# Kernel optimization log

Measured on AMD Instinct MI355X. Metric: run time of the kernel, lower is better.

Reference implementation:

```python
import jax, jax.numpy as jnp
import numpy as np

B = 16          # graphs per batch
N_PER = 1024    # coarse points per graph
M_PER = 4096    # fine (skip) points per graph
K = 3           # knn neighbors
NVEC = 64       # number of l=1 (vector) reps -> F = 3*NVEC
F = 3 * NVEC
F_SKIP = 64
HID = 256
OUT = 128
N = B * N_PER
M = B * M_PER


def _random_rotations(key, n):
    # QR of gaussian -> orthonormal local frames [n,3,3]
    q, _ = jnp.linalg.qr(jax.random.normal(key, (n, 3, 3), dtype=jnp.float32))
    return q


def setup_inputs() -> dict:
    key = jax.random.key(0)
    ks = jax.random.split(key, 10)
    x = jax.random.normal(ks[0], (N, F), dtype=jnp.float32)
    pos = jax.random.normal(ks[1], (N, 3), dtype=jnp.float32)
    pos_skip = jax.random.normal(ks[2], (M, 3), dtype=jnp.float32)
    x_skip = jax.random.normal(ks[3], (M, F_SKIP), dtype=jnp.float32)
    lframes = _random_rotations(ks[4], N)
    lframes_skip = _random_rotations(ks[5], M)
    W1 = jax.random.normal(ks[6], (F + F_SKIP, HID), dtype=jnp.float32) * 0.05
    b1 = jnp.zeros((HID,), dtype=jnp.float32)
    W2 = jax.random.normal(ks[7], (HID, OUT), dtype=jnp.float32) * 0.05
    b2 = jnp.zeros((OUT,), dtype=jnp.float32)
    batch = jnp.repeat(jnp.arange(B, dtype=jnp.int64), N_PER)
    batch_skip = jnp.repeat(jnp.arange(B, dtype=jnp.int64), M_PER)
    return dict(x=x, pos=pos, pos_skip=pos_skip, x_skip=x_skip,
                lframes=lframes, lframes_skip=lframes_skip,
                W1=W1, b1=b1, W2=W2, b2=b2,
                batch=batch, batch_skip=batch_skip)


def _knn_indices(pos, pos_skip):
    # Uniform per-example batching: knn of fine points (queries) among coarse points.
    px = pos.reshape(B, N_PER, 3)       # source points
    py = pos_skip.reshape(B, M_PER, 3)  # query points
    # squared distances via ||y||^2 + ||x||^2 - 2 y.x (only used for ranking)
    d2 = ((py * py).sum(-1)[:, :, None]
          + (px * px).sum(-1)[:, None, :]
          - 2.0 * jnp.einsum('bmd,bnd->bmn', py, px))  # [B, M_PER, N_PER]
    _, idx = jax.lax.top_k(-d2, K)                     # [B, M_PER, K] local indices
    # globalize indices (batch offset)
    x_idx = (idx + (jnp.arange(B) * N_PER)[:, None, None]).reshape(M, K)
    return x_idx


def reference(x, pos, pos_skip, x_skip, lframes, lframes_skip,
              W1, b1, W2, b2, batch, batch_skip):
    x_idx = _knn_indices(pos, pos_skip)                 # [M, K]

    # exact squared distances on gathered neighbors (matches torch diff*diff path)
    diff = pos[x_idx] - pos_skip[:, None, :]            # [M, K, 3]
    sqd = (diff * diff).sum(-1)                         # [M, K]
    w = 1.0 / jnp.maximum(sqd, 1e-16)                   # [M, K]

    # change of local frames: U = R_end @ R_start^T, per edge
    Rx = lframes[x_idx]                                 # [M, K, 3, 3]
    Ry = lframes_skip                                   # [M, 3, 3]
    U = jnp.einsum('mab,mkcb->mkac', Ry, Rx)            # [M, K, 3, 3]

    # transform features (NVEC vector reps) into the target frame
    xv = x[x_idx].reshape(M, K, NVEC, 3)                # gathered edge features
    xt = jnp.einsum('mkab,mkvb->mkva', U, xv)           # [M, K, NVEC, 3]

    # weighted mean over the K neighbors (== scatter-sum / scatter-sum, since
    # each target node has exactly K incoming edges)
    num = (xt * w[:, :, None, None]).sum(axis=1)        # [M, NVEC, 3]
    den = w.sum(axis=1)[:, None, None]                  # [M, 1, 1]
    y = (num / den).reshape(M, F)

    h = jnp.concatenate([y, x_skip], axis=-1)           # [M, F + F_SKIP]
    out = jax.nn.relu(h @ W1 + b1) @ W2 + b2            # [M, OUT]
    return (out, pos_skip, batch_skip, lframes_skip)
```

## Files before the change

### kernel.cpp

```cpp
#include <hip/hip_runtime.h>
#include <hip/hip_bf16.h>

#define B_GR   16
#define N_PER  1024
#define M_PER  4096
#define NVEC   64
#define FDIM   192
#define FSKIP  64
#define HID    256
#define ODIM   128
#define N_TOT  (B_GR * N_PER)
#define M_TOT  (B_GR * M_PER)

typedef __attribute__((ext_vector_type(8))) short short8v;
typedef __attribute__((ext_vector_type(4))) float f32x4;

__device__ __forceinline__ unsigned short f2bf(float f) {
    __hip_bfloat16 h = __float2bfloat16(f);
    return *reinterpret_cast<unsigned short*>(&h);
}

__device__ __forceinline__ int hsw(int r, int e) {
    return r * 256 + (e ^ ((r & 7) << 3));
}

__global__ __launch_bounds__(256) void wprep_kernel(
    const float* __restrict__ W1, const float* __restrict__ W2,
    unsigned short* __restrict__ wt1, unsigned short* __restrict__ wt2)
{
    const int i = blockIdx.x * 256 + threadIdx.x;
    if (i < 256 * 256) {
        const int k = i >> 8, c = i & 255;
        wt1[c * 256 + k] = f2bf(W1[i]);
    } else {
        const int j = i - 256 * 256;
        const int k = j >> 7, c = j & 127;
        wt2[c * 256 + k] = f2bf(W2[j]);
    }
}

__global__ __launch_bounds__(512, 2) void fused_kernel(
    const float* __restrict__ x,
    const float* __restrict__ pos,
    const float* __restrict__ pos_skip,
    const float* __restrict__ x_skip,
    const float* __restrict__ lframes,
    const float* __restrict__ lframes_skip,
    const unsigned short* __restrict__ wt1,
    const float* __restrict__ b1,
    const unsigned short* __restrict__ wt2,
    const float* __restrict__ b2,
    float* __restrict__ out)
{
    __shared__ __align__(16) char smraw[64 * 256 * 2];
    __shared__ __align__(16) float Usc[64 * 28];
    __shared__ int idxL[64 * 3];

    float4*         pc = reinterpret_cast<float4*>(smraw);
    unsigned short* hb = reinterpret_cast<unsigned short*>(smraw);

    const int tid  = threadIdx.x;
    const int lane = tid & 63;
    const int wv   = tid >> 6;
    const int raw  = blockIdx.x;
    const int blk  = (raw & 7) * 128 + (raw >> 3);
    const int lo   = lane & 15;
    const int hi   = lane >> 4;
    const int b    = blk >> 6;

    #pragma unroll
    for (int k = 0; k < 2; ++k) {
        const int j = tid + k * 512;
        const float* p = pos + (size_t)(b * N_PER + j) * 3;
        float a0 = p[0], a1 = p[1], a2 = p[2];
        pc[j] = make_float4(a0, a1, a2, a0*a0 + a1*a1 + a2*a2);
    }
    __syncthreads();

    {
        const int q   = tid >> 3;
        const int sub = tid & 7;
        const int m   = blk * 64 + q;
        float nqx, nqy, nqz, qq;
        {
            const float qx = pos_skip[m*3+0], qy = pos_skip[m*3+1],
                        qz = pos_skip[m*3+2];
            qq  = qx*qx + qy*qy + qz*qz;
            nqx = -2.0f*qx; nqy = -2.0f*qy; nqz = -2.0f*qz;
        }

        float d0 = 1e30f, d1 = 1e30f, d2 = 1e30f;
        int   i0 = 0,     i1 = 0,     i2 = 0;
        float e0 = 1e30f, e1 = 1e30f, e2 = 1e30f;
        int   k0 = 0,     k1 = 0,     k2 = 0;
        #pragma unroll 4
        for (int t = 0; t < 64; ++t) {
            const int ja = t*16 + sub;
            const int jb = ja + 8;
            float4 ca = pc[ja];
            float4 cb = pc[jb];
            float ra = fmaf(nqx, ca.x, fmaf(nqy, ca.y, fmaf(nqz, ca.z, qq + ca.w)));
            float rb = fmaf(nqx, cb.x, fmaf(nqy, cb.y, fmaf(nqz, cb.z, qq + cb.w)));
            {
                bool c0 = ra < d0, c1 = ra < d1, c2 = ra < d2;
                i2 = c2 ? (c1 ? i1 : ja) : i2;
                i1 = c1 ? (c0 ? i0 : ja) : i1;
                i0 = c0 ? ja : i0;
                d2 = c2 ? (c1 ? d1 : ra) : d2;
                d1 = c1 ? (c0 ? d0 : ra) : d1;
                d0 = c0 ? ra : d0;
            }
            {
                bool c0 = rb < e0, c1 = rb < e1, c2 = rb < e2;
                k2 = c2 ? (c1 ? k1 : jb) : k2;
                k1 = c1 ? (c0 ? k0 : jb) : k1;
                k0 = c0 ? jb : k0;
                e2 = c2 ? (c1 ? e1 : rb) : e2;
                e1 = c1 ? (c0 ? e0 : rb) : e1;
                e0 = c0 ? rb : e0;
            }
        }
        {
            const float ee[3] = {e0, e1, e2};
            const int   jj[3] = {k0, k1, k2};
            #pragma unroll
            for (int s = 0; s < 3; ++s) {
                const float e = ee[s]; const int j = jj[s];
                bool c0 = (e < d0) || (e == d0 && j < i0);
                bool c1 = (e < d1) || (e == d1 && j < i1);
                bool c2 = (e < d2) || (e == d2 && j < i2);
                i2 = c2 ? (c1 ? i1 : j) : i2;
                i1 = c1 ? (c0 ? i0 : j) : i1;
                i0 = c0 ? j : i0;
                d2 = c2 ? (c1 ? d1 : e) : d2;
                d1 = c1 ? (c0 ? d0 : e) : d1;
                d0 = c0 ? e : d0;
            }
        }
        #pragma unroll
        for (int mask = 1; mask <= 4; mask <<= 1) {
            float f0 = __shfl_xor(d0, mask), f1 = __shfl_xor(d1, mask),
                  f2 = __shfl_xor(d2, mask);
            int   j0 = __shfl_xor(i0, mask), j1 = __shfl_xor(i1, mask),
                  j2 = __shfl_xor(i2, mask);
            const float ee[3] = {f0, f1, f2};
            const int   jj[3] = {j0, j1, j2};
            #pragma unroll
            for (int s = 0; s < 3; ++s) {
                const float e = ee[s]; const int j = jj[s];
                bool c0 = (e < d0) || (e == d0 && j < i0);
                bool c1 = (e < d1) || (e == d1 && j < i1);
                bool c2 = (e < d2) || (e == d2 && j < i2);
                i2 = c2 ? (c1 ? i1 : j) : i2;
                i1 = c1 ? (c0 ? i0 : j) : i1;
                i0 = c0 ? j : i0;
                d2 = c2 ? (c1 ? d1 : e) : d2;
                d1 = c1 ? (c0 ? d0 : e) : d1;
                d0 = c0 ? e : d0;
            }
        }

        if (sub < 3) {
            const int jl = (sub == 0) ? i0 : (sub == 1) ? i1 : i2;
            idxL[q*3 + sub] = jl;

            const float qx = -0.5f*nqx, qy = -0.5f*nqy, qz = -0.5f*nqz;
            float w[3];
            const int jls[3] = {i0, i1, i2};
            #pragma unroll
            for (int s = 0; s < 3; ++s) {
                float4 c = pc[jls[s]];
                float dx = c.x - qx, dy = c.y - qy, dz = c.z - qz;
                w[s] = 1.0f / fmaxf(dx*dx + dy*dy + dz*dz, 1e-16f);
            }
            const float wsub = (sub == 0) ? w[0] : (sub == 1) ? w[1] : w[2];
            const float sS   = wsub / (w[0] + w[1] + w[2]);
            const int   nb   = b * N_PER + jl;

            float RyS[9], Rx[9];
            #pragma unroll
            for (int t = 0; t < 9; ++t) RyS[t] = sS * lframes_skip[(size_t)m*9 + t];
            #pragma unroll
            for (int t = 0; t < 9; ++t) Rx[t] = lframes[(size_t)nb*9 + t];

            float* dst = &Usc[q*28 + sub*9];
            #pragma unroll
            for (int a = 0; a < 3; ++a)
                #pragma unroll
                for (int c = 0; c < 3; ++c)
                    dst[a*3+c] = RyS[a*3+0]*Rx[c*3+0]
                               + RyS[a*3+1]*Rx[c*3+1]
                               + RyS[a*3+2]*Rx[c*3+2];
        }
    }

    if (wv >= 4) {
        #pragma unroll
        for (int rr = 0; rr < 8; ++rr) {
            const int r = wv * 8 + rr;
            const int m = blk * 64 + r;
            hb[hsw(r, 192+lane)] = f2bf(x_skip[(size_t)m*FSKIP + lane]);
        }
    }
    __syncthreads();

    for (int rr = 0; rr < 8; ++rr) {
        const int r = wv * 8 + rr;
        const int m = blk * 64 + r;
        const int nbs[3] = {b*N_PER + idxL[r*3+0],
                            b*N_PER + idxL[r*3+1],
                            b*N_PER + idxL[r*3+2]};

        float Ub[28];
        float4* Ub4 = reinterpret_cast<float4*>(Ub);
        #pragma unroll
        for (int t = 0; t < 7; ++t)
            Ub4[t] = *reinterpret_cast<const float4*>(&Usc[r*28 + t*4]);

        float n0 = 0.f, n1 = 0.f, n2 = 0.f;
        #pragma unroll
        for (int k = 0; k < 3; ++k) {
            const float* xp = x + (size_t)nbs[k]*FDIM + lane*3;
            const float v0 = xp[0], v1 = xp[1], v2 = xp[2];
            const int o = k*9;
            n0 += Ub[o+0]*v0 + Ub[o+1]*v1 + Ub[o+2]*v2;
            n1 += Ub[o+3]*v0 + Ub[o+4]*v1 + Ub[o+5]*v2;
            n2 += Ub[o+6]*v0 + Ub[o+7]*v1 + Ub[o+8]*v2;
        }
        hb[hsw(r, lane*3+0)] = f2bf(n0);
        hb[hsw(r, lane*3+1)] = f2bf(n1);
        hb[hsw(r, lane*3+2)] = f2bf(n2);
        if (wv < 4)
            hb[hsw(r, 192+lane)] = f2bf(x_skip[(size_t)m*FSKIP + lane]);
    }
    __syncthreads();

    f32x4 acc[4][2];
    #pragma unroll
    for (int fi = 0; fi < 4; ++fi)
        #pragma unroll
        for (int ci = 0; ci < 2; ++ci) acc[fi][ci] = (f32x4)0.f;

    for (int ks = 0; ks < 8; ++ks) {
        const int kk = ks*32 + hi*8;
        short8v a[4], bf[2];
        #pragma unroll
        for (int fi = 0; fi < 4; ++fi) {
            const int r = fi*16 + lo;
            a[fi] = *reinterpret_cast<const short8v*>(
                &hb[r*256 + (kk ^ ((lo & 7) << 3))]);
        }
        #pragma unroll
        for (int ci = 0; ci < 2; ++ci) {
            const int cb = wv*32 + ci*16 + lo;
            bf[ci] = *reinterpret_cast<const short8v*>(&wt1[cb*256 + kk]);
        }
        #pragma unroll
        for (int fi = 0; fi < 4; ++fi)
            #pragma unroll
            for (int ci = 0; ci < 2; ++ci)
                acc[fi][ci] = __builtin_amdgcn_mfma_f32_16x16x32_bf16(
                    a[fi], bf[ci], acc[fi][ci], 0, 0, 0);
    }
    __syncthreads();

    {
        float b1v[2];
        #pragma unroll
        for (int ci = 0; ci < 2; ++ci) b1v[ci] = b1[wv*32 + ci*16 + lo];
        #pragma unroll
        for (int fi = 0; fi < 4; ++fi)
            #pragma unroll
            for (int ci = 0; ci < 2; ++ci)
                #pragma unroll
                for (int q = 0; q < 4; ++q) {
                    const int r = fi*16 + hi*4 + q;
                    const int c = wv*32 + ci*16 + lo;
                    hb[hsw(r, c)] = f2bf(fmaxf(acc[fi][ci][q] + b1v[ci], 0.f));
                }
    }
    __syncthreads();

    f32x4 acc2[4];
    #pragma unroll
    for (int fi = 0; fi < 4; ++fi) acc2[fi] = (f32x4)0.f;

    for (int ks = 0; ks < 8; ++ks) {
        const int kk = ks*32 + hi*8;
        short8v a[4], bf;
        #pragma unroll
        for (int fi = 0; fi < 4; ++fi) {
            const int r = fi*16 + lo;
            a[fi] = *reinterpret_cast<const short8v*>(
                &hb[r*256 + (kk ^ ((lo & 7) << 3))]);
        }
        {
            const int cb = wv*16 + lo;
            bf = *reinterpret_cast<const short8v*>(&wt2[cb*256 + kk]);
        }
        #pragma unroll
        for (int fi = 0; fi < 4; ++fi)
            acc2[fi] = __builtin_amdgcn_mfma_f32_16x16x32_bf16(
                a[fi], bf, acc2[fi], 0, 0, 0);
    }

    {
        const float b2v = b2[wv*16 + lo];
        #pragma unroll
        for (int fi = 0; fi < 4; ++fi)
            #pragma unroll
            for (int q = 0; q < 4; ++q) {
                const int r = fi*16 + hi*4 + q;
                const int c = wv*16 + lo;
                out[(size_t)(blk*64 + r)*ODIM + c] = acc2[fi][q] + b2v;
            }
    }
}

__global__ __launch_bounds__(256) void tail_kernel(
    const float* __restrict__ pos_skip,
    const int*   __restrict__ batch_skip,
    const float* __restrict__ lframes_skip,
    float* __restrict__ dst)
{
    const int i = blockIdx.x * 256 + threadIdx.x;
    const int P = M_TOT * 3;
    const int Q = P + M_TOT;
    const int R = Q + M_TOT * 9;
    if (i < P)      dst[i] = pos_skip[i];
    else if (i < Q) dst[i] = (float)batch_skip[i - P];
    else if (i < R) dst[i] = lframes_skip[i - Q];
}

extern "C" void kernel_launch(void* const* d_in, const int* in_sizes, int n_in,
                              void* d_out, int out_size, void* d_ws, size_t ws_size,
                              hipStream_t stream) {
    const float* x            = (const float*)d_in[0];
    const float* pos          = (const float*)d_in[1];
    const float* pos_skip     = (const float*)d_in[2];
    const float* x_skip       = (const float*)d_in[3];
    const float* lframes      = (const float*)d_in[4];
    const float* lframes_skip = (const float*)d_in[5];
    const float* W1           = (const float*)d_in[6];
    const float* b1           = (const float*)d_in[7];
    const float* W2           = (const float*)d_in[8];
    const float* b2           = (const float*)d_in[9];
    const int*   batch_skip   = (const int*)d_in[11];

    char* ws = (char*)d_ws;
    unsigned short* wt1 = (unsigned short*)ws;
    unsigned short* wt2 = (unsigned short*)(ws + 131072);
    float* out = (float*)d_out;

    wprep_kernel<<<(256*256 + 256*128) / 256, 256, 0, stream>>>(W1, W2, wt1, wt2);

    fused_kernel<<<M_TOT/64, 512, 0, stream>>>(x, pos, pos_skip, x_skip,
                                               lframes, lframes_skip,
                                               wt1, b1, wt2, b2, out);

    float* tail = out + (size_t)M_TOT * ODIM;
    const int tail_elems = M_TOT * (3 + 1 + 9);
    tail_kernel<<<(tail_elems + 255)/256, 256, 0, stream>>>(
        pos_skip, batch_skip, lframes_skip, tail);
}
```

Baseline: 72.05 us.

## Precompute packed float4 positions globally and read KNN candidates from cache

The prep kernel now also writes each coarse point as a float4 (xyz plus squared norm) into workspace. The fused kernel reads KNN candidates straight from global/L1 instead of staging them in shared memory, which removes one barrier and the aliasing between the position buffer and the bf16 activation tile. x_skip is now written into the activation tile by every wave at kernel start, dropping the split between waves. The risk is that the inner KNN loop now depends on global/cache load latency instead of LDS reads.

```diff
diff --git a/kernel.cpp b/kernel.cpp
--- a/kernel.cpp
+++ b/kernel.cpp
@@ -26,22 +26,29 @@
 
 __global__ __launch_bounds__(256) void wprep_kernel(
     const float* __restrict__ W1, const float* __restrict__ W2,
-    unsigned short* __restrict__ wt1, unsigned short* __restrict__ wt2)
+    const float* __restrict__ pos,
+    unsigned short* __restrict__ wt1, unsigned short* __restrict__ wt2,
+    float4* __restrict__ pos4)
 {
     const int i = blockIdx.x * 256 + threadIdx.x;
-    if (i < 256 * 256) {
+    if (i < 65536) {
         const int k = i >> 8, c = i & 255;
         wt1[c * 256 + k] = f2bf(W1[i]);
-    } else {
-        const int j = i - 256 * 256;
+    } else if (i < 98304) {
+        const int j = i - 65536;
         const int k = j >> 7, c = j & 127;
         wt2[c * 256 + k] = f2bf(W2[j]);
+    } else {
+        const int p = i - 98304;
+        const float* pp = pos + (size_t)p * 3;
+        float a0 = pp[0], a1 = pp[1], a2 = pp[2];
+        pos4[p] = make_float4(a0, a1, a2, a0*a0 + a1*a1 + a2*a2);
     }
 }
 
 __global__ __launch_bounds__(512, 2) void fused_kernel(
     const float* __restrict__ x,
-    const float* __restrict__ pos,
+    const float4* __restrict__ pos4,
     const float* __restrict__ pos_skip,
     const float* __restrict__ x_skip,
     const float* __restrict__ lframes,
@@ -52,12 +59,9 @@
     const float* __restrict__ b2,
     float* __restrict__ out)
 {
-    __shared__ __align__(16) char smraw[64 * 256 * 2];
+    __shared__ __align__(16) unsigned short hb[64 * 256];
     __shared__ __align__(16) float Usc[64 * 28];
     __shared__ int idxL[64 * 3];
-
-    float4*         pc = reinterpret_cast<float4*>(smraw);
-    unsigned short* hb = reinterpret_cast<unsigned short*>(smraw);
 
     const int tid  = threadIdx.x;
     const int lane = tid & 63;
@@ -68,14 +72,14 @@
     const int hi   = lane >> 4;
     const int b    = blk >> 6;
 
+    const float4* __restrict__ gp4 = pos4 + (size_t)b * N_PER;
+
     #pragma unroll
-    for (int k = 0; k < 2; ++k) {
-        const int j = tid + k * 512;
-        const float* p = pos + (size_t)(b * N_PER + j) * 3;
-        float a0 = p[0], a1 = p[1], a2 = p[2];
-        pc[j] = make_float4(a0, a1, a2, a0*a0 + a1*a1 + a2*a2);
-    }
-    __syncthreads();
+    for (int rr = 0; rr < 8; ++rr) {
+        const int r = wv * 8 + rr;
+        const int m = blk * 64 + r;
+        hb[hsw(r, 192+lane)] = f2bf(x_skip[(size_t)m*FSKIP + lane]);
+    }
 
     {
         const int q   = tid >> 3;
@@ -97,8 +101,8 @@
         for (int t = 0; t < 64; ++t) {
             const int ja = t*16 + sub;
             const int jb = ja + 8;
-            float4 ca = pc[ja];
-            float4 cb = pc[jb];
+            float4 ca = gp4[ja];
+            float4 cb = gp4[jb];
             float ra = fmaf(nqx, ca.x, fmaf(nqy, ca.y, fmaf(nqz, ca.z, qq + ca.w)));
             float rb = fmaf(nqx, cb.x, fmaf(nqy, cb.y, fmaf(nqz, cb.z, qq + cb.w)));
             {
@@ -169,7 +173,7 @@
             const int jls[3] = {i0, i1, i2};
             #pragma unroll
             for (int s = 0; s < 3; ++s) {
-                float4 c = pc[jls[s]];
+                float4 c = gp4[jls[s]];
                 float dx = c.x - qx, dy = c.y - qy, dz = c.z - qz;
                 w[s] = 1.0f / fmaxf(dx*dx + dy*dy + dz*dz, 1e-16f);
             }
@@ -194,19 +198,8 @@
         }
     }
 
-    if (wv >= 4) {
-        #pragma unroll
-        for (int rr = 0; rr < 8; ++rr) {
-            const int r = wv * 8 + rr;
-            const int m = blk * 64 + r;
-            hb[hsw(r, 192+lane)] = f2bf(x_skip[(size_t)m*FSKIP + lane]);
-        }
-    }
-    __syncthreads();
-
     for (int rr = 0; rr < 8; ++rr) {
         const int r = wv * 8 + rr;
-        const int m = blk * 64 + r;
         const int nbs[3] = {b*N_PER + idxL[r*3+0],
                             b*N_PER + idxL[r*3+1],
                             b*N_PER + idxL[r*3+2]};
@@ -230,8 +223,6 @@
         hb[hsw(r, lane*3+0)] = f2bf(n0);
         hb[hsw(r, lane*3+1)] = f2bf(n1);
         hb[hsw(r, lane*3+2)] = f2bf(n2);
-        if (wv < 4)
-            hb[hsw(r, 192+lane)] = f2bf(x_skip[(size_t)m*FSKIP + lane]);
     }
     __syncthreads();
 
@@ -348,13 +339,14 @@
     const int*   batch_skip   = (const int*)d_in[11];
 
     char* ws = (char*)d_ws;
-    unsigned short* wt1 = (unsigned short*)ws;
-    unsigned short* wt2 = (unsigned short*)(ws + 131072);
+    unsigned short* wt1  = (unsigned short*)ws;
+    unsigned short* wt2  = (unsigned short*)(ws + 131072);
+    float4*         pos4 = (float4*)(ws + 131072 + 65536);
     float* out = (float*)d_out;
 
-    wprep_kernel<<<(256*256 + 256*128) / 256, 256, 0, stream>>>(W1, W2, wt1, wt2);
-
-    fused_kernel<<<M_TOT/64, 512, 0, stream>>>(x, pos, pos_skip, x_skip,
+    wprep_kernel<<<448, 256, 0, stream>>>(W1, W2, pos, wt1, wt2, pos4);
+
+    fused_kernel<<<M_TOT/64, 512, 0, stream>>>(x, pos4, pos_skip, x_skip,
                                                lframes, lframes_skip,
                                                wt1, b1, wt2, b2, out);
 
```

New measurement: 83.53 us. +15.9%, slower.
